# Kernel tuning notes

Measured on AMD Instinct MI355X. Metric: run time of the kernel, lower is better.

## Reference

```python
import jax, jax.numpy as jnp
import numpy as np


def setup_inputs() -> dict:
    key = jax.random.key(0)
    ks = jax.random.split(key, 4)
    B, C, H, W = 4, 256, 64, 64
    Cq = C // 8
    s_in = 1.0 / np.sqrt(C)
    return {
        "x": jax.random.normal(ks[0], (B, C, H, W), dtype=jnp.float32),
        "Wq": jax.random.normal(ks[1], (Cq, C), dtype=jnp.float32) * s_in,
        "bq": jnp.zeros((Cq,), dtype=jnp.float32),
        "Wk": jax.random.normal(ks[2], (Cq, C), dtype=jnp.float32) * s_in,
        "bk": jnp.zeros((Cq,), dtype=jnp.float32),
        "Wv": jax.random.normal(ks[3], (C, C), dtype=jnp.float32) * s_in,
        "bv": jnp.zeros((C,), dtype=jnp.float32),
    }


def reference(x, Wq, bq, Wk, bk, Wv, bv):
    B, C, H, W = x.shape
    N = H * W
    xf = x.reshape(B, C, N)  # [B, C, N] tokens
    # 1x1 convs == per-token linear projections
    Q = jnp.einsum('qc,bcn->bqn', Wq, xf) + bq[None, :, None]  # [B, C/8, N]
    K = jnp.einsum('qc,bcn->bqn', Wk, xf) + bk[None, :, None]  # [B, C/8, N]
    V = jnp.einsum('vc,bcn->bvn', Wv, xf) + bv[None, :, None]  # [B, C,   N]
    # full self-attention over spatial tokens (no scaling, per original)
    scores = jnp.einsum('bdi,bdj->bij', Q, K)      # [B, N, N]
    attn = jax.nn.softmax(scores, axis=-1)
    out = jnp.einsum('bcj,bij->bci', V, attn)       # [B, C, N]
    return out.reshape(B, C, H, W) + x
```

## Files before the change

### kernel.cpp

```cpp
#include <hip/hip_runtime.h>

typedef short short8 __attribute__((ext_vector_type(8)));
typedef float f32x4 __attribute__((ext_vector_type(4)));
typedef float f32x16 __attribute__((ext_vector_type(16)));
typedef unsigned short u16;
typedef u16 u16x8 __attribute__((ext_vector_type(8)));
typedef unsigned int u32;
typedef u32 u32x4 __attribute__((ext_vector_type(4)));

#define NTOK 4096
#define CDIM 256
#define TJ 64
#define NJT 32
#define LOG2E 1.44269504088896f

__device__ __forceinline__ u16 f2bf(float f) {
    unsigned u = __float_as_uint(f);
    unsigned r = (u + 0x7fffu + ((u >> 16) & 1u)) >> 16;
    return (u16)r;
}
__device__ __forceinline__ float bf2f(u16 h) { return __uint_as_float(((unsigned)h) << 16); }
__device__ __forceinline__ u32 pk_bf16(float a, float b) {
    u32 w;
    asm("v_cvt_pk_bf16_f32 %0, %1, %2" : "=v"(w) : "v"(a), "v"(b));
    return w;
}

__global__ __launch_bounds__(256)
void wconv(const float* __restrict__ Wq, const float* __restrict__ Wk,
           const float* __restrict__ Wv, u16* __restrict__ whi, u16* __restrict__ wlo) {
    const int row = blockIdx.x;
    const int col = threadIdx.x;
    float v;
    if (row < 32)       v = Wq[row * 256 + col];
    else if (row < 64)  v = Wk[(row - 32) * 256 + col];
    else                v = Wv[(row - 64) * 256 + col];
    u16 h = f2bf(v);
    whi[row * 256 + col] = h;
    wlo[row * 256 + col] = f2bf(v - bf2f(h));
}

__global__ __launch_bounds__(256, 1)
void proj_fused(const float* __restrict__ x,
                const u16* __restrict__ whi, const u16* __restrict__ wlo,
                const float* __restrict__ bq, const float* __restrict__ bk,
                const float* __restrict__ bv,
                u16* __restrict__ qhi, u16* __restrict__ qlo,
                u16* __restrict__ khi, u16* __restrict__ klo,
                u16* __restrict__ vbf) {
    __shared__ __attribute__((aligned(16))) u16 lxh[64][260];
    __shared__ __attribute__((aligned(16))) u16 lxl[64][260];
    const int b  = blockIdx.y;
    const int n0 = blockIdx.x * 64;
    const int t  = threadIdx.x;
    const int w  = t >> 6;
    const int l  = t & 63;
    const int cl = l & 15;
    const int kg = l >> 4;

    const int sn = (t & 15) * 4;
    const int sc = t >> 4;
#pragma unroll
    for (int cc = 0; cc < 16; cc++) {
        const int c = sc + cc * 16;
        const f32x4 xv = *(const f32x4*)&x[((size_t)(b * CDIM + c)) * NTOK + n0 + sn];
#pragma unroll
        for (int i = 0; i < 4; i++) {
            u16 hh = f2bf(xv[i]);
            lxh[sn + i][c] = hh;
            lxl[sn + i][c] = f2bf(xv[i] - bf2f(hh));
        }
    }
    __syncthreads();

    f32x4 acc[5][4];
    const f32x4 fz = {0.f, 0.f, 0.f, 0.f};
#pragma unroll
    for (int i = 0; i < 5; i++)
#pragma unroll
        for (int nt = 0; nt < 4; nt++) acc[i][nt] = fz;

#pragma unroll 2
    for (int ks = 0; ks < 8; ks++) {
        const int k0 = ks * 32;
        short8 bh[4], bl[4];
#pragma unroll
        for (int nt = 0; nt < 4; nt++) {
            bh[nt] = *(const short8*)&lxh[nt * 16 + cl][k0 + kg * 8];
            bl[nt] = *(const short8*)&lxl[nt * 16 + cl][k0 + kg * 8];
        }
#pragma unroll
        for (int i = 0; i < 5; i++) {
            const int mt = w * 5 + i;
            const size_t wb = (size_t)(mt * 16 + cl) * 256 + k0 + kg * 8;
            const short8 ah = *(const short8*)&whi[wb];
            const short8 al = *(const short8*)&wlo[wb];
#pragma unroll
            for (int nt = 0; nt < 4; nt++) {
                acc[i][nt] = __builtin_amdgcn_mfma_f32_16x16x32_bf16(ah, bh[nt], acc[i][nt], 0, 0, 0);
                acc[i][nt] = __builtin_amdgcn_mfma_f32_16x16x32_bf16(ah, bl[nt], acc[i][nt], 0, 0, 0);
                acc[i][nt] = __builtin_amdgcn_mfma_f32_16x16x32_bf16(al, bh[nt], acc[i][nt], 0, 0, 0);
            }
        }
    }

#pragma unroll
    for (int i = 0; i < 5; i++) {
        const int mt = w * 5 + i;
#pragma unroll
        for (int nt = 0; nt < 4; nt++) {
            const int n = n0 + nt * 16 + cl;
#pragma unroll
            for (int r = 0; r < 4; r++) {
                const int m = kg * 4 + r;
                float v = acc[i][nt][r];
                if (mt < 2) {
                    const int ch = mt * 16 + m;
                    v += bq[ch];
                    u16 hh = f2bf(v);
                    qhi[((size_t)(b * NTOK + n)) * 32 + ch] = hh;
                    qlo[((size_t)(b * NTOK + n)) * 32 + ch] = f2bf(v - bf2f(hh));
                } else if (mt < 4) {
                    const int ch = (mt - 2) * 16 + m;
                    v += bk[ch];
                    u16 hh = f2bf(v);
                    khi[((size_t)(b * NTOK + n)) * 32 + ch] = hh;
                    klo[((size_t)(b * NTOK + n)) * 32 + ch] = f2bf(v - bf2f(hh));
                } else {
                    const int c2 = (mt - 4) * 16 + m;
                    vbf[((size_t)(b * CDIM + c2)) * NTOK + n] = f2bf(v + bv[c2]);
                }
            }
        }
    }
}

__global__ __launch_bounds__(256, 2)
void attn_part(const u16* __restrict__ qhi, const u16* __restrict__ qlo,
               const u16* __restrict__ khi, const u16* __restrict__ klo,
               const u16* __restrict__ vbf,
               float* __restrict__ pacc, float* __restrict__ pl) {
    __shared__ __attribute__((aligned(16))) u16 lkh[2][TJ][32];
    __shared__ __attribute__((aligned(16))) u16 lkl[2][TJ][32];
    __shared__ __attribute__((aligned(16))) u16 lv[2][128][72];
    float (*lt)[32][33] = reinterpret_cast<float (*)[32][33]>(&lv[0][0][0]);

    const int lin = blockIdx.x;
    const int p   = lin & 7;
    const int b   = p >> 1;
    const int h   = p & 1;
    const int js  = (lin >> 3) & 1;
    const int qb  = lin >> 4;
    const int i0  = qb * 128;
    const int jb  = js * 2048;
    const int t   = threadIdx.x;
    const int w   = t >> 6;
    const int l   = t & 63;
    const int q5  = l & 31;
    const int hi  = l >> 5;

    const int iq = i0 + w * 32 + q5;
    const size_t qbase = ((size_t)(b * NTOK + iq)) * 32;
    const short8 qh0 = *(const short8*)&qhi[qbase + hi * 8];
    const short8 qh1 = *(const short8*)&qhi[qbase + 16 + hi * 8];
    const short8 ql0 = *(const short8*)&qlo[qbase + hi * 8];
    const short8 ql1 = *(const short8*)&qlo[qbase + 16 + hi * 8];

    const int vc   = t & 127;
    const int vch0 = (t >> 7) * 4;
    const u16* vsrc = &vbf[((size_t)(b * CDIM + h * 128 + vc)) * NTOK];
    const int kj   = (t & 127) >> 1;
    const int kch2 = (t & 1) * 2;
    const u16* ksrcbase = (t < 128) ? khi : klo;
    const u16* ksrc = &ksrcbase[((size_t)(b * NTOK + kj)) * 32 + kch2 * 8];

    u16x8 vreg[4];
    u16x8 kreg0, kreg1;

    auto stage_load = [&](int tt) {
        const size_t j0 = (size_t)(jb + tt * TJ);
#pragma unroll
        for (int i = 0; i < 4; i++)
            vreg[i] = *(const u16x8*)&vsrc[j0 + (vch0 + i) * 8];
        kreg0 = *(const u16x8*)&ksrc[j0 * 32];
        kreg1 = *(const u16x8*)&ksrc[j0 * 32 + 8];
    };
    auto stage_write = [&](int buf) {
        const int s2 = (vc >> 2) & 3;
#pragma unroll
        for (int i = 0; i < 4; i++) {
            const int ci = vch0 + i;
            const int ps = (ci & 4) | ((ci ^ s2) & 3);
            *(u16x8*)&lv[buf][vc][ps * 8] = vreg[i];
        }
        const int swk = (kj >> 2) & 3;
        u16* kbase = (t < 128) ? &lkh[buf][kj][0] : &lkl[buf][kj][0];
        *(u16x8*)&kbase[((kch2)     ^ swk) * 8] = kreg0;
        *(u16x8*)&kbase[((kch2 + 1) ^ swk) * 8] = kreg1;
    };

    f32x16 acc0, acc1, acc2, acc3;
#pragma unroll
    for (int i = 0; i < 16; i++) { acc0[i] = 0.f; acc1[i] = 0.f; acc2[i] = 0.f; acc3[i] = 0.f; }
    float l_r = 0.f;

    auto qkt32 = [&](int cur, int jt) -> f32x16 {
        f32x16 s;
#pragma unroll
        for (int i = 0; i < 16; i++) s[i] = 0.f;
        const int row = jt * 32 + q5;
        const int sw  = (row >> 2) & 3;
        {
            const int ph = ((0 * 2 + hi) ^ sw) * 8;
            short8 kh = *(const short8*)&lkh[cur][row][ph];
            short8 kl = *(const short8*)&lkl[cur][row][ph];
            s = __builtin_amdgcn_mfma_f32_32x32x16_bf16(kh, qh0, s, 0, 0, 0);
            s = __builtin_amdgcn_mfma_f32_32x32x16_bf16(kl, qh0, s, 0, 0, 0);
            s = __builtin_amdgcn_mfma_f32_32x32x16_bf16(kh, ql0, s, 0, 0, 0);
        }
        {
            const int ph = ((1 * 2 + hi) ^ sw) * 8;
            short8 kh = *(const short8*)&lkh[cur][row][ph];
            short8 kl = *(const short8*)&lkl[cur][row][ph];
            s = __builtin_amdgcn_mfma_f32_32x32x16_bf16(kh, qh1, s, 0, 0, 0);
            s = __builtin_amdgcn_mfma_f32_32x32x16_bf16(kl, qh1, s, 0, 0, 0);
            s = __builtin_amdgcn_mfma_f32_32x32x16_bf16(kh, ql1, s, 0, 0, 0);
        }
        return s;
    };

    auto mkfrag = [&](u32 own0, u32 own1, u32 own2, u32 own3) -> short8 {
        const u32 sendA = hi ? own0 : own2;
        const u32 sendB = hi ? own1 : own3;
        const u32 recvA = (u32)__shfl_xor((int)sendA, 32);
        const u32 recvB = (u32)__shfl_xor((int)sendB, 32);
        u32x4 bw;
        bw[0] = hi ? recvA : own0;
        bw[1] = hi ? recvB : own1;
        bw[2] = hi ? own2 : recvA;
        bw[3] = hi ? own3 : recvB;
        return __builtin_bit_cast(short8, bw);
    };

    stage_load(0);
    stage_write(0);
    __syncthreads();

#pragma unroll 2
    for (int tt = 0; tt < NJT; ++tt) {
        const int cur = tt & 1;
        const int nxt = cur ^ 1;
        const bool pre = (tt + 1 < NJT);
        if (pre) stage_load(tt + 1);

        __builtin_amdgcn_s_setprio(1);
        f32x16 s0 = qkt32(cur, 0);
        f32x16 s1 = qkt32(cur, 1);
        __builtin_amdgcn_s_setprio(0);

#pragma unroll
        for (int i = 0; i < 16; i++) {
            s0[i] = exp2f(s0[i] * LOG2E);
            s1[i] = exp2f(s1[i] * LOG2E);
        }
        float psum = 0.f;
#pragma unroll
        for (int i = 0; i < 16; i++) psum += s0[i] + s1[i];
        l_r += psum;

        short8 pf0 = mkfrag(pk_bf16(s0[0],  s0[1]),  pk_bf16(s0[2],  s0[3]),
                            pk_bf16(s0[4],  s0[5]),  pk_bf16(s0[6],  s0[7]));
        short8 pf1 = mkfrag(pk_bf16(s0[8],  s0[9]),  pk_bf16(s0[10], s0[11]),
                            pk_bf16(s0[12], s0[13]), pk_bf16(s0[14], s0[15]));
        short8 pf2 = mkfrag(pk_bf16(s1[0],  s1[1]),  pk_bf16(s1[2],  s1[3]),
                            pk_bf16(s1[4],  s1[5]),  pk_bf16(s1[6],  s1[7]));
        short8 pf3 = mkfrag(pk_bf16(s1[8],  s1[9]),  pk_bf16(s1[10], s1[11]),
                            pk_bf16(s1[12], s1[13]), pk_bf16(s1[14], s1[15]));

        __builtin_amdgcn_s_setprio(1);
#pragma unroll
        for (int jg = 0; jg < 4; jg++) {
            const int ch = jg * 2 + hi;
            const short8 pf = (jg == 0) ? pf0 : (jg == 1) ? pf1 : (jg == 2) ? pf2 : pf3;
#define PV_CT(CT, ACC)                                                        \
            {                                                                 \
                const int row = CT * 32 + q5;                                 \
                const int sw  = (row >> 2) & 3;                               \
                const int ph  = ((ch & 4) | ((ch ^ sw) & 3)) * 8;             \
                short8 vb = *(const short8*)&lv[cur][row][ph];                \
                ACC = __builtin_amdgcn_mfma_f32_32x32x16_bf16(vb, pf, ACC, 0, 0, 0); \
            }
            PV_CT(0, acc0)
            PV_CT(1, acc1)
            PV_CT(2, acc2)
            PV_CT(3, acc3)
#undef PV_CT
        }
        __builtin_amdgcn_s_setprio(0);

        if (pre) stage_write(nxt);
        __syncthreads();
    }

    l_r += __shfl_xor(l_r, 32);
    if (h == 0 && l < 32)
        pl[((size_t)((b * 2 + js) * 32 + qb)) * 128 + w * 32 + q5] = l_r;

    const size_t tile = (size_t)(((b * 2 + h) * 2 + js) * 32 + qb);
    const int r2 = l >> 1;
    const int qc = (l & 1) * 16;
#pragma unroll
    for (int ct = 0; ct < 4; ct++) {
        const f32x16 a = (ct == 0) ? acc0 : (ct == 1) ? acc1 : (ct == 2) ? acc2 : acc3;
#pragma unroll
        for (int reg = 0; reg < 16; reg++) {
            const int crow = (reg & 3) + 8 * (reg >> 2) + 4 * hi;
            lt[w][crow][q5] = a[reg];
        }
        const int c_local = ct * 32 + r2;
        const size_t base = (tile * 128 + c_local) * 128 + w * 32 + qc;
#pragma unroll
        for (int m4 = 0; m4 < 4; m4++) {
            const f32x4 vv = *(const f32x4*)&lt[w][r2][qc + m4 * 4];
            *(f32x4*)&pacc[base + m4 * 4] = vv;
        }
    }
}

__global__ __launch_bounds__(256)
void attn_combine(const float* __restrict__ pacc, const float* __restrict__ pl,
                  const float* __restrict__ x, float* __restrict__ out) {
    const int g = blockIdx.x * 256 + threadIdx.x;
#pragma unroll
    for (int rep = 0; rep < 4; rep++) {
        const int f = g + rep * 262144;
        const int il4 = f & 31;
        const int qb  = (f >> 5) & 31;
        const int c   = (f >> 10) & 255;
        const int b   = f >> 18;
        const int h   = c >> 7;
        const int cl7 = c & 127;
        const size_t t0 = (size_t)(((b * 2 + h) * 2 + 0) * 32 + qb);
        const size_t t1 = t0 + 32;
        const f32x4 a0 = *(const f32x4*)&pacc[(t0 * 128 + cl7) * 128 + il4 * 4];
        const f32x4 a1 = *(const f32x4*)&pacc[(t1 * 128 + cl7) * 128 + il4 * 4];
        const f32x4 l0 = *(const f32x4*)&pl[((size_t)((b * 2 + 0) * 32 + qb)) * 128 + il4 * 4];
        const f32x4 l1 = *(const f32x4*)&pl[((size_t)((b * 2 + 1) * 32 + qb)) * 128 + il4 * 4];
        const size_t ox = ((size_t)(b * 256 + c) * 4096) + qb * 128 + il4 * 4;
        const f32x4 xv = *(const f32x4*)&x[ox];
        f32x4 o;
#pragma unroll
        for (int i = 0; i < 4; i++)
            o[i] = (a0[i] + a1[i]) / (l0[i] + l1[i]) + xv[i];
        *(f32x4*)&out[ox] = o;
    }
}

extern "C" void kernel_launch(void* const* d_in, const int* in_sizes, int n_in,
                              void* d_out, int out_size, void* d_ws, size_t ws_size,
                              hipStream_t stream) {
    const float* x  = (const float*)d_in[0];
    const float* Wq = (const float*)d_in[1];
    const float* bq = (const float*)d_in[2];
    const float* Wk = (const float*)d_in[3];
    const float* bk = (const float*)d_in[4];
    const float* Wv = (const float*)d_in[5];
    const float* bv = (const float*)d_in[6];
    float* out = (float*)d_out;

    u16* qhi = (u16*)d_ws;
    u16* qlo = qhi + (size_t)4 * NTOK * 32;
    u16* khi = qlo + (size_t)4 * NTOK * 32;
    u16* klo = khi + (size_t)4 * NTOK * 32;
    u16* vbf = klo + (size_t)4 * NTOK * 32;
    u16* whi = vbf + (size_t)4 * CDIM * NTOK;
    u16* wlo = whi + (size_t)320 * 256;
    float* pacc = (float*)(wlo + (size_t)320 * 256);
    float* pl   = pacc + (size_t)512 * 128 * 128;

    wconv<<<dim3(320), 256, 0, stream>>>(Wq, Wk, Wv, whi, wlo);
    proj_fused<<<dim3(64, 4), 256, 0, stream>>>(x, whi, wlo, bq, bk, bv,
                                                qhi, qlo, khi, klo, vbf);
    attn_part<<<dim3(512), 256, 0, stream>>>(qhi, qlo, khi, klo, vbf, pacc, pl);
    attn_combine<<<dim3(1024), 256, 0, stream>>>(pacc, pl, x, out);
}
```

Before: 135.8 us.

## Use 512-thread attention blocks with 256 queries and four-way key split

The attention kernel now runs 8 waves per block covering 256 query rows, which shares each K/V LDS tile across twice as many queries. The key range is split four ways instead of two, so each block iterates over 16 key tiles. Cooperative loading is redistributed across the larger thread count, and the combine kernel sums four partials instead of two. This doubles the partial-accumulator workspace and the traffic through the combine step, and raises per-CU register and LDS pressure from the larger blocks.

Result: slower. 146.5 us (+8.0%).

```diff
diff --git a/kernel.cpp b/kernel.cpp
--- a/kernel.cpp
+++ b/kernel.cpp
@@ -11,7 +11,7 @@
 #define NTOK 4096
 #define CDIM 256
 #define TJ 64
-#define NJT 32
+#define NJT 16
 #define LOG2E 1.44269504088896f
 
 __device__ __forceinline__ u16 f2bf(float f) {
@@ -135,7 +135,7 @@
     }
 }
 
-__global__ __launch_bounds__(256, 2)
+__global__ __launch_bounds__(512, 2)
 void attn_part(const u16* __restrict__ qhi, const u16* __restrict__ qlo,
                const u16* __restrict__ khi, const u16* __restrict__ klo,
                const u16* __restrict__ vbf,
@@ -149,10 +149,10 @@
     const int p   = lin & 7;
     const int b   = p >> 1;
     const int h   = p & 1;
-    const int js  = (lin >> 3) & 1;
-    const int qb  = lin >> 4;
-    const int i0  = qb * 128;
-    const int jb  = js * 2048;
+    const int js  = (lin >> 3) & 3;
+    const int qp  = lin >> 5;
+    const int i0  = qp * 256;
+    const int jb  = js * 1024;
     const int t   = threadIdx.x;
     const int w   = t >> 6;
     const int l   = t & 63;
@@ -167,36 +167,33 @@
     const short8 ql1 = *(const short8*)&qlo[qbase + 16 + hi * 8];
 
     const int vc   = t & 127;
-    const int vch0 = (t >> 7) * 4;
+    const int vch0 = (t >> 7) * 2;
     const u16* vsrc = &vbf[((size_t)(b * CDIM + h * 128 + vc)) * NTOK];
-    const int kj   = (t & 127) >> 1;
-    const int kch2 = (t & 1) * 2;
-    const u16* ksrcbase = (t < 128) ? khi : klo;
-    const u16* ksrc = &ksrcbase[((size_t)(b * NTOK + kj)) * 32 + kch2 * 8];
-
-    u16x8 vreg[4];
-    u16x8 kreg0, kreg1;
+    const int tk  = t & 255;
+    const int kj  = tk >> 2;
+    const int kch = tk & 3;
+    const u16* ksrcbase = (t < 256) ? khi : klo;
+    const u16* ksrc = &ksrcbase[((size_t)(b * NTOK + kj)) * 32 + kch * 8];
+
+    u16x8 vreg0, vreg1, kreg;
 
     auto stage_load = [&](int tt) {
         const size_t j0 = (size_t)(jb + tt * TJ);
-#pragma unroll
-        for (int i = 0; i < 4; i++)
-            vreg[i] = *(const u16x8*)&vsrc[j0 + (vch0 + i) * 8];
-        kreg0 = *(const u16x8*)&ksrc[j0 * 32];
-        kreg1 = *(const u16x8*)&ksrc[j0 * 32 + 8];
+        vreg0 = *(const u16x8*)&vsrc[j0 + (vch0)     * 8];
+        vreg1 = *(const u16x8*)&vsrc[j0 + (vch0 + 1) * 8];
+        kreg  = *(const u16x8*)&ksrc[j0 * 32];
     };
     auto stage_write = [&](int buf) {
         const int s2 = (vc >> 2) & 3;
-#pragma unroll
-        for (int i = 0; i < 4; i++) {
-            const int ci = vch0 + i;
-            const int ps = (ci & 4) | ((ci ^ s2) & 3);
-            *(u16x8*)&lv[buf][vc][ps * 8] = vreg[i];
-        }
-        const int swk = (kj >> 2) & 3;
-        u16* kbase = (t < 128) ? &lkh[buf][kj][0] : &lkl[buf][kj][0];
-        *(u16x8*)&kbase[((kch2)     ^ swk) * 8] = kreg0;
-        *(u16x8*)&kbase[((kch2 + 1) ^ swk) * 8] = kreg1;
+        const int c0 = vch0;
+        const int c1 = vch0 + 1;
+        const int p0 = (c0 & 4) | ((c0 ^ s2) & 3);
+        const int p1 = (c1 & 4) | ((c1 ^ s2) & 3);
+        *(u16x8*)&lv[buf][vc][p0 * 8] = vreg0;
+        *(u16x8*)&lv[buf][vc][p1 * 8] = vreg1;
+        const int ph = kch ^ ((kj >> 2) & 3);
+        u16* kbase = (t < 256) ? &lkh[buf][kj][0] : &lkl[buf][kj][0];
+        *(u16x8*)&kbase[ph * 8] = kreg;
     };
 
     f32x16 acc0, acc1, acc2, acc3;
@@ -304,9 +301,9 @@
 
     l_r += __shfl_xor(l_r, 32);
     if (h == 0 && l < 32)
-        pl[((size_t)((b * 2 + js) * 32 + qb)) * 128 + w * 32 + q5] = l_r;
-
-    const size_t tile = (size_t)(((b * 2 + h) * 2 + js) * 32 + qb);
+        pl[((size_t)(b * 4 + js)) * NTOK + i0 + w * 32 + q5] = l_r;
+
+    const size_t tile = (size_t)(((b * 2 + h) * 4 + js) * 16 + qp);
     const int r2 = l >> 1;
     const int qc = (l & 1) * 16;
 #pragma unroll
@@ -318,7 +315,7 @@
             lt[w][crow][q5] = a[reg];
         }
         const int c_local = ct * 32 + r2;
-        const size_t base = (tile * 128 + c_local) * 128 + w * 32 + qc;
+        const size_t base = (tile * 128 + c_local) * 256 + w * 32 + qc;
 #pragma unroll
         for (int m4 = 0; m4 < 4; m4++) {
             const f32x4 vv = *(const f32x4*)&lt[w][r2][qc + m4 * 4];
@@ -334,24 +331,27 @@
 #pragma unroll
     for (int rep = 0; rep < 4; rep++) {
         const int f = g + rep * 262144;
-        const int il4 = f & 31;
-        const int qb  = (f >> 5) & 31;
+        const int qi4 = f & 63;
+        const int qp  = (f >> 6) & 15;
         const int c   = (f >> 10) & 255;
         const int b   = f >> 18;
         const int h   = c >> 7;
         const int cl7 = c & 127;
-        const size_t t0 = (size_t)(((b * 2 + h) * 2 + 0) * 32 + qb);
-        const size_t t1 = t0 + 32;
-        const f32x4 a0 = *(const f32x4*)&pacc[(t0 * 128 + cl7) * 128 + il4 * 4];
-        const f32x4 a1 = *(const f32x4*)&pacc[(t1 * 128 + cl7) * 128 + il4 * 4];
-        const f32x4 l0 = *(const f32x4*)&pl[((size_t)((b * 2 + 0) * 32 + qb)) * 128 + il4 * 4];
-        const f32x4 l1 = *(const f32x4*)&pl[((size_t)((b * 2 + 1) * 32 + qb)) * 128 + il4 * 4];
-        const size_t ox = ((size_t)(b * 256 + c) * 4096) + qb * 128 + il4 * 4;
+        f32x4 asum = {0.f, 0.f, 0.f, 0.f};
+        f32x4 lsum = {0.f, 0.f, 0.f, 0.f};
+#pragma unroll
+        for (int js = 0; js < 4; js++) {
+            const size_t tile = (size_t)(((b * 2 + h) * 4 + js) * 16 + qp);
+            const f32x4 a = *(const f32x4*)&pacc[(tile * 128 + cl7) * 256 + qi4 * 4];
+            const f32x4 lv4 = *(const f32x4*)&pl[((size_t)(b * 4 + js)) * 4096 + qp * 256 + qi4 * 4];
+#pragma unroll
+            for (int i = 0; i < 4; i++) { asum[i] += a[i]; lsum[i] += lv4[i]; }
+        }
+        const size_t ox = ((size_t)(b * 256 + c)) * 4096 + qp * 256 + qi4 * 4;
         const f32x4 xv = *(const f32x4*)&x[ox];
         f32x4 o;
 #pragma unroll
-        for (int i = 0; i < 4; i++)
-            o[i] = (a0[i] + a1[i]) / (l0[i] + l1[i]) + xv[i];
+        for (int i = 0; i < 4; i++) o[i] = asum[i] / lsum[i] + xv[i];
         *(f32x4*)&out[ox] = o;
     }
 }
@@ -376,11 +376,11 @@
     u16* whi = vbf + (size_t)4 * CDIM * NTOK;
     u16* wlo = whi + (size_t)320 * 256;
     float* pacc = (float*)(wlo + (size_t)320 * 256);
-    float* pl   = pacc + (size_t)512 * 128 * 128;
+    float* pl   = pacc + (size_t)512 * 128 * 256;
 
     wconv<<<dim3(320), 256, 0, stream>>>(Wq, Wk, Wv, whi, wlo);
     proj_fused<<<dim3(64, 4), 256, 0, stream>>>(x, whi, wlo, bq, bk, bv,
                                                 qhi, qlo, khi, klo, vbf);
-    attn_part<<<dim3(512), 256, 0, stream>>>(qhi, qlo, khi, klo, vbf, pacc, pl);
+    attn_part<<<dim3(512), 512, 0, stream>>>(qhi, qlo, khi, klo, vbf, pacc, pl);
     attn_combine<<<dim3(1024), 256, 0, stream>>>(pacc, pl, x, out);
 }
```
